# Kernel optimization log

Hardware: AMD Instinct MI355X
Metric: run time of the kernel (lower is better)

## Reference

```python
import jax, jax.numpy as jnp
import numpy as np

N_NODES = 50000
IN_CH = 128
HIDDEN = 64
OUT = 32
HEADS = 4


def _gat_conv(x, src, dst, W, a_src, a_dst, b, heads, ch, concat):
    """PyG-style GATConv (eval mode, self-loops already in src/dst)."""
    N = x.shape[0]
    h = (x @ W).reshape(N, heads, ch)                      # [N,H,C]
    asrc = jnp.einsum('nhc,hc->nh', h, a_src)              # [N,H]
    adst = jnp.einsum('nhc,hc->nh', h, a_dst)              # [N,H]
    e = jax.nn.leaky_relu(asrc[src] + adst[dst], 0.2)      # [E,H]
    # segment softmax over edges grouped by destination node
    m = jax.ops.segment_max(e, dst, num_segments=N)        # [N,H]
    e = jnp.exp(e - m[dst])
    z = jax.ops.segment_sum(e, dst, num_segments=N)        # [N,H]
    alpha = e / (z[dst] + 1e-16)                           # [E,H]
    out = jax.ops.segment_sum(h[src] * alpha[:, :, None], dst, num_segments=N)  # [N,H,C]
    out = out.reshape(N, heads * ch) if concat else out.mean(axis=1)
    return out + b


def _layer_norm(x, g, b):
    mu = x.mean(axis=-1, keepdims=True)
    var = ((x - mu) ** 2).mean(axis=-1, keepdims=True)
    return (x - mu) * jax.lax.rsqrt(var + 1e-5) * g + b


def setup_inputs() -> dict:
    key = jax.random.key(0)
    ks = jax.random.split(key, 20)
    HID = HEADS * HIDDEN  # 256
    s = 0.1
    inp = {
        'x': jax.random.normal(ks[0], (N_NODES, IN_CH), jnp.float32),
        'edge_index': jax.random.randint(ks[1], (2, 800000), 0, N_NODES, jnp.int64 if jax.config.jax_enable_x64 else jnp.int32),
        # conv1
        'W1': jax.random.normal(ks[2], (IN_CH, HID), jnp.float32) * s,
        'a1_src': jax.random.normal(ks[3], (HEADS, HIDDEN), jnp.float32) * s,
        'a1_dst': jax.random.normal(ks[4], (HEADS, HIDDEN), jnp.float32) * s,
        'b1': jnp.zeros((HID,), jnp.float32),
        'g1': jnp.ones((HID,), jnp.float32),
        'be1': jnp.zeros((HID,), jnp.float32),
        # conv2
        'W2': jax.random.normal(ks[5], (HID, HID), jnp.float32) * s,
        'a2_src': jax.random.normal(ks[6], (HEADS, HIDDEN), jnp.float32) * s,
        'a2_dst': jax.random.normal(ks[7], (HEADS, HIDDEN), jnp.float32) * s,
        'b2': jnp.zeros((HID,), jnp.float32),
        'g2': jnp.ones((HID,), jnp.float32),
        'be2': jnp.zeros((HID,), jnp.float32),
        # conv3 (heads=1)
        'W3': jax.random.normal(ks[8], (HID, OUT), jnp.float32) * s,
        'a3_src': jax.random.normal(ks[9], (1, OUT), jnp.float32) * s,
        'a3_dst': jax.random.normal(ks[10], (1, OUT), jnp.float32) * s,
        'b3': jnp.zeros((OUT,), jnp.float32),
    }
    return inp


def reference(x, edge_index, W1, a1_src, a1_dst, b1, g1, be1,
              W2, a2_src, a2_dst, b2, g2, be2,
              W3, a3_src, a3_dst, b3):
    N = x.shape[0]
    loops = jnp.arange(N, dtype=edge_index.dtype)
    ei = jnp.concatenate([edge_index, jnp.stack([loops, loops])], axis=1)
    src, dst = ei[0], ei[1]
    h = _gat_conv(x, src, dst, W1, a1_src, a1_dst, b1, HEADS, HIDDEN, True)
    h = jax.nn.elu(_layer_norm(h, g1, be1))
    h = _gat_conv(h, src, dst, W2, a2_src, a2_dst, b2, HEADS, HIDDEN, True)
    h = jax.nn.elu(_layer_norm(h, g2, be2))
    return _gat_conv(h, src, dst, W3, a3_src, a3_dst, b3, 1, OUT, True)
```

## Files before the change

### kernel.cpp

```cpp
#include <hip/hip_runtime.h>
#include <math.h>

#define NN 50000

typedef __attribute__((ext_vector_type(8))) short bf16x8;
typedef __attribute__((ext_vector_type(4))) float f32x4;

__device__ inline float wred_max(float v){
  #pragma unroll
  for(int s=32;s>0;s>>=1) v=fmaxf(v,__shfl_xor(v,s,64));
  return v;
}
__device__ inline float wred_sum(float v){
  #pragma unroll
  for(int s=32;s>0;s>>=1) v+=__shfl_xor(v,s,64);
  return v;
}
__device__ inline float lrelu(float x){ return x>0.f? x : 0.2f*x; }
__device__ inline float rlf(float v,int l){ return __int_as_float(__builtin_amdgcn_readlane(__float_as_int(v),l)); }

__device__ inline ushort f2bf(float f){
  union{float f;unsigned u;} v; v.f=f;
  unsigned u=v.u;
  return (ushort)((u + 0x7fffu + ((u>>16)&1u)) >> 16);
}
__device__ inline float bflo(unsigned u){ return __uint_as_float(u<<16); }
__device__ inline float bfhi(unsigned u){ return __uint_as_float(u&0xffff0000u); }

__global__ void casttr_k(const float* __restrict__ W, ushort* __restrict__ Wt, int K, int N){
  int i=blockIdx.x*blockDim.x+threadIdx.x;
  if(i<K*N){ int k=i/N, n=i%N; Wt[n*K+k]=f2bf(W[i]); }
}

__global__ void hist_k(const int* __restrict__ dstA,int* __restrict__ counts,int E){
  int i=blockIdx.x*blockDim.x+threadIdx.x;
  if(i<E) atomicAdd(&counts[dstA[i]],1);
}

__global__ __launch_bounds__(1024) void scan1_k(const int* __restrict__ counts,int* __restrict__ offs,
                                                int* __restrict__ bsum,int N){
  __shared__ int stot[16];
  int t=threadIdx.x; int lane=t&63, wv=t>>6;
  int base=blockIdx.x*1024;
  int orig=(base+t<N)?counts[base+t]:0;
  int v=orig;
  #pragma unroll
  for(int s=1;s<64;s<<=1){ int u=__shfl_up(v,s,64); if(lane>=s) v+=u; }
  if(lane==63) stot[wv]=v;
  __syncthreads();
  if(wv==0){
    int tv=(lane<16)?stot[lane]:0;
    #pragma unroll
    for(int s=1;s<16;s<<=1){ int u=__shfl_up(tv,s,64); if(lane>=s) tv+=u; }
    if(lane<16) stot[lane]=tv;
  }
  __syncthreads();
  int wpref=(wv>0)?stot[wv-1]:0;
  if(base+t<N) offs[base+t]=wpref+v-orig;
  if(t==1023) bsum[blockIdx.x]=stot[15];
}
__global__ void scan2_k(int* __restrict__ bsum,int NB){
  int lane=threadIdx.x;
  int v=(lane<NB)?bsum[lane]:0;
  int incl=v;
  #pragma unroll
  for(int s=1;s<64;s<<=1){ int u=__shfl_up(incl,s,64); if(lane>=s) incl+=u; }
  if(lane<NB) bsum[lane]=incl-v;
}
__global__ __launch_bounds__(1024) void scan3_k(int* __restrict__ offs,const int* __restrict__ bsum,int N,int E){
  int i=blockIdx.x*1024+threadIdx.x;
  if(i<N) offs[i]+=bsum[blockIdx.x];
  if(i==N-1) offs[N]=E;
}

__global__ void scatter_k(const int* __restrict__ srcA,const int* __restrict__ dstA,
                          const int* __restrict__ offs,int* cur,int* __restrict__ ssrc,int E){
  int i=blockIdx.x*blockDim.x+threadIdx.x;
  if(i<E){ int d=dstA[i]; int p=offs[d]+atomicAdd(&cur[d],1); ssrc[p]=srcA[i]; }
}

template<int WR,int WC,int MI,int NI,int DOTM,int AF32>
__global__ __launch_bounds__(256,2) void gemm_bf16_k(const void* __restrict__ Av,
    const ushort* __restrict__ Bt, ushort* __restrict__ C,
    const float* __restrict__ aS, const float* __restrict__ aD,
    float* __restrict__ as_, float* __restrict__ ad_,
    int M, int N, int K){
  constexpr int BM = WR*MI*16;
  constexpr int BN = WC*NI*16;
  constexpr int LDK = 40;
  __shared__ ushort sA[BM*LDK];
  __shared__ ushort sB[BN*LDK];
  int tid=threadIdx.x;
  int lane=tid&63, w=tid>>6;
  int wr=w/WC, wc=w%WC;
  int bm=blockIdx.y*BM, bn=blockIdx.x*BN;
  f32x4 acc[MI][NI]={};

  for(int k0=0;k0<K;k0+=32){
    if constexpr (AF32){
      const float* A=(const float*)Av;
      #pragma unroll
      for(int i=0;i<(BM*8)/256;i++){
        int c=tid+i*256;
        int r=c>>3, cc=c&7;
        int gr=bm+r;
        float4 v={0.f,0.f,0.f,0.f};
        if(gr<M) v=*(const float4*)(A+(size_t)gr*K+k0+cc*4);
        unsigned long long p=(unsigned long long)f2bf(v.x)
          |((unsigned long long)f2bf(v.y)<<16)
          |((unsigned long long)f2bf(v.z)<<32)
          |((unsigned long long)f2bf(v.w)<<48);
        *(unsigned long long*)(sA+r*LDK+cc*4)=p;
      }
    } else {
      const ushort* A=(const ushort*)Av;
      #pragma unroll
      for(int i=0;i<(BM*4)/256;i++){
        int c=tid+i*256;
        int r=c>>2, cc=c&3;
        int gr=bm+r;
        ulonglong2 v; v.x=0; v.y=0;
        if(gr<M) v=*(const ulonglong2*)(A+(size_t)gr*K+k0+cc*8);
        *(ulonglong2*)(sA+r*LDK+cc*8)=v;
      }
    }
    if constexpr ((BN*4)>=256){
      #pragma unroll
      for(int i=0;i<(BN*4)/256;i++){
        int c=tid+i*256;
        int r=c>>2, cc=c&3;
        ulonglong2 v=*(const ulonglong2*)(Bt+(size_t)(bn+r)*K+k0+cc*8);
        *(ulonglong2*)(sB+r*LDK+cc*8)=v;
      }
    } else {
      if(tid<BN*4){
        int r=tid>>2, cc=tid&3;
        ulonglong2 v=*(const ulonglong2*)(Bt+(size_t)(bn+r)*K+k0+cc*8);
        *(ulonglong2*)(sB+r*LDK+cc*8)=v;
      }
    }
    __syncthreads();
    bf16x8 af[MI], bf[NI];
    #pragma unroll
    for(int m=0;m<MI;m++)
      af[m]=*(bf16x8*)(sA+((wr*MI+m)*16+(lane&15))*LDK+(lane>>4)*8);
    #pragma unroll
    for(int n=0;n<NI;n++)
      bf[n]=*(bf16x8*)(sB+((wc*NI+n)*16+(lane&15))*LDK+(lane>>4)*8);
    #pragma unroll
    for(int m=0;m<MI;m++)
      #pragma unroll
      for(int n=0;n<NI;n++)
        acc[m][n]=__builtin_amdgcn_mfma_f32_16x16x32_bf16(af[m],bf[n],acc[m][n],0,0,0);
    __syncthreads();
  }
  int rb=lane>>4, cl=lane&15;
  float av[NI], dv[NI];
  #pragma unroll
  for(int n=0;n<NI;n++){
    int gc=bn+(wc*NI+n)*16+cl;
    if constexpr (DOTM!=0){ av[n]=aS[gc]; dv[n]=aD[gc]; }
    else { av[n]=0.f; dv[n]=0.f; }
  }
  #pragma unroll
  for(int m=0;m<MI;m++){
    #pragma unroll
    for(int i=0;i<4;i++){
      int gr=bm+(wr*MI+m)*16+rb*4+i;
      if constexpr (DOTM==1){
        int h=(bn>>6)+wc;
        float ps=0.f,pd=0.f;
        #pragma unroll
        for(int n=0;n<NI;n++){ ps+=acc[m][n][i]*av[n]; pd+=acc[m][n][i]*dv[n]; }
        #pragma unroll
        for(int msk=1;msk<16;msk<<=1){
          ps+=__shfl_xor(ps,msk,64); pd+=__shfl_xor(pd,msk,64);
        }
        if(cl==0 && gr<M){ as_[gr*4+h]=ps; ad_[gr*4+h]=pd; }
      } else if constexpr (DOTM==2){
        float ps=0.f,pd=0.f;
        #pragma unroll
        for(int n=0;n<NI;n++){ ps+=acc[m][n][i]*av[n]; pd+=acc[m][n][i]*dv[n]; }
        #pragma unroll
        for(int msk=1;msk<16;msk<<=1){
          ps+=__shfl_xor(ps,msk,64); pd+=__shfl_xor(pd,msk,64);
        }
        if(cl==0 && gr<M){ as_[gr]=ps; ad_[gr]=pd; }
      }
      if(gr<M){
        #pragma unroll
        for(int n=0;n<NI;n++){
          int gc=bn+(wc*NI+n)*16+cl;
          int pos = (DOTM==1) ? (4*(gc&63)+(gc>>6)) : gc;
          C[(size_t)gr*N+pos]=f2bf(acc[m][n][i]);
        }
      }
    }
  }
}

__global__ __launch_bounds__(256) void agg4_k(const ushort* __restrict__ hb,
    const float* __restrict__ as_,const float* __restrict__ ad_,
    const int* __restrict__ offs,const int* __restrict__ ssrc,
    const float* __restrict__ bias,const float* __restrict__ g,const float* __restrict__ be,
    ushort* __restrict__ outb,int N){
  int lane=threadIdx.x&63, wv=threadIdx.x>>6;
  int n=blockIdx.x*4+wv; if(n>=N) return;
  int lane4=lane*4;
  float ad[4], es[4];
  #pragma unroll
  for(int k=0;k<4;k++) ad[k]=ad_[n*4+k];
  #pragma unroll
  for(int k=0;k<4;k++) es[k]=lrelu(as_[n*4+k]+ad[k]);
  int o0=offs[n],o1=offs[n+1];
  int cnt=o1-o0;
  float m[4], inv[4], acc[4];

  if(cnt<=64){
    int sv=0;
    float lv[4]={-1e30f,-1e30f,-1e30f,-1e30f};
    if(lane<cnt){
      sv=ssrc[o0+lane];
      float4 avv=*(const float4*)(as_+(size_t)sv*4);
      lv[0]=lrelu(avv.x+ad[0]); lv[1]=lrelu(avv.y+ad[1]);
      lv[2]=lrelu(avv.z+ad[2]); lv[3]=lrelu(avv.w+ad[3]);
    }
    #pragma unroll
    for(int k=0;k<4;k++) m[k]=fmaxf(es[k],wred_max(lv[k]));
    float w4[4];
    #pragma unroll
    for(int k=0;k<4;k++) w4[k]=(lane<cnt)?__expf(lv[k]-m[k]):0.f;
    #pragma unroll
    for(int k=0;k<4;k++){
      float z=wred_sum(w4[k])+__expf(es[k]-m[k]);
      inv[k]=1.f/(z+1e-16f);
    }
    #pragma unroll
    for(int k=0;k<4;k++) w4[k]*=inv[k];
    {
      uint2 u=*(const uint2*)(hb+(size_t)n*256+lane4);
      float hv[4]={bflo(u.x),bfhi(u.x),bflo(u.y),bfhi(u.y)};
      #pragma unroll
      for(int k=0;k<4;k++) acc[k]=__expf(es[k]-m[k])*inv[k]*hv[k];
    }
    int cnt8=(cnt+7)&~7;
    uint2 uA[8];
    #pragma unroll
    for(int i=0;i<8;i++){
      int s=__builtin_amdgcn_readlane(sv,i);
      uA[i]=*(const uint2*)(hb+(size_t)s*256+lane4);
    }
    for(int t=0;t<cnt8;t+=8){
      uint2 uB[8];
      if(t+8<cnt8){
        #pragma unroll
        for(int i=0;i<8;i++){
          int s=__builtin_amdgcn_readlane(sv,t+8+i);
          uB[i]=*(const uint2*)(hb+(size_t)s*256+lane4);
        }
      }
      #pragma unroll
      for(int i=0;i<8;i++){
        acc[0]+=rlf(w4[0],t+i)*bflo(uA[i].x);
        acc[1]+=rlf(w4[1],t+i)*bfhi(uA[i].x);
        acc[2]+=rlf(w4[2],t+i)*bflo(uA[i].y);
        acc[3]+=rlf(w4[3],t+i)*bfhi(uA[i].y);
      }
      #pragma unroll
      for(int i=0;i<8;i++) uA[i]=uB[i];
    }
  } else {
    #pragma unroll
    for(int k=0;k<4;k++) m[k]=es[k];
    {
      float lm[4]={-1e30f,-1e30f,-1e30f,-1e30f};
      for(int j=o0+lane;j<o1;j+=64){
        int s=ssrc[j];
        float4 avv=*(const float4*)(as_+(size_t)s*4);
        float a[4]={avv.x,avv.y,avv.z,avv.w};
        #pragma unroll
        for(int k=0;k<4;k++) lm[k]=fmaxf(lm[k],lrelu(a[k]+ad[k]));
      }
      #pragma unroll
      for(int k=0;k<4;k++) m[k]=fmaxf(m[k],wred_max(lm[k]));
    }
    {
      float lz[4]={0.f,0.f,0.f,0.f};
      for(int j=o0+lane;j<o1;j+=64){
        int s=ssrc[j];
        float4 avv=*(const float4*)(as_+(size_t)s*4);
        float a[4]={avv.x,avv.y,avv.z,avv.w};
        #pragma unroll
        for(int k=0;k<4;k++) lz[k]+=__expf(lrelu(a[k]+ad[k])-m[k]);
      }
      #pragma unroll
      for(int k=0;k<4;k++){
        float z=wred_sum(lz[k])+__expf(es[k]-m[k]);
        inv[k]=1.f/(z+1e-16f);
      }
    }
    {
      uint2 u=*(const uint2*)(hb+(size_t)n*256+lane4);
      float hv[4]={bflo(u.x),bfhi(u.x),bflo(u.y),bfhi(u.y)};
      #pragma unroll
      for(int k=0;k<4;k++) acc[k]=__expf(es[k]-m[k])*inv[k]*hv[k];
    }
    for(int base=o0;base<o1;base+=64){
      int c2=min(64,o1-base);
      int j=base+lane;
      int sv=0; float w4[4]={0.f,0.f,0.f,0.f};
      if(j<o1){
        sv=ssrc[j];
        float4 avv=*(const float4*)(as_+(size_t)sv*4);
        float a[4]={avv.x,avv.y,avv.z,avv.w};
        #pragma unroll
        for(int k=0;k<4;k++) w4[k]=__expf(lrelu(a[k]+ad[k])-m[k])*inv[k];
      }
      for(int t=0;t<c2;t++){
        int s=__builtin_amdgcn_readlane(sv,t);
        uint2 u=*(const uint2*)(hb+(size_t)s*256+lane4);
        acc[0]+=rlf(w4[0],t)*bflo(u.x);
        acc[1]+=rlf(w4[1],t)*bfhi(u.x);
        acc[2]+=rlf(w4[2],t)*bflo(u.y);
        acc[3]+=rlf(w4[3],t)*bfhi(u.y);
      }
    }
  }
  #pragma unroll
  for(int k=0;k<4;k++) acc[k]+=bias[k*64+lane];
  float tot=wred_sum(acc[0]+acc[1]+acc[2]+acc[3]);
  float mu=tot*(1.f/256.f);
  float vs=0.f;
  #pragma unroll
  for(int k=0;k<4;k++){ float d=acc[k]-mu; vs+=d*d; }
  float var=wred_sum(vs)*(1.f/256.f);
  float r=rsqrtf(var+1e-5f);
  #pragma unroll
  for(int k=0;k<4;k++){
    float v=(acc[k]-mu)*r*g[k*64+lane]+be[k*64+lane];
    float ev= v>0.f? v : expm1f(v);
    outb[(size_t)n*256+k*64+lane]=f2bf(ev);
  }
}

__global__ __launch_bounds__(256) void agg1_k(const ushort* __restrict__ hb,
    const float* __restrict__ as_,const float* __restrict__ ad_,
    const int* __restrict__ offs,const int* __restrict__ ssrc,
    const float* __restrict__ bias,float* __restrict__ out,int N){
  int lane=threadIdx.x&63, wv=threadIdx.x>>6;
  int n=blockIdx.x*4+wv; if(n>=N) return;
  float ad=ad_[n];
  float es=lrelu(as_[n]+ad);
  int o0=offs[n],o1=offs[n+1];
  int cnt=o1-o0;
  float m, inv, acc=0.f;

  if(cnt<=64){
    int sv=0; float lv=-1e30f;
    if(lane<cnt){ sv=ssrc[o0+lane]; lv=lrelu(as_[sv]+ad); }
    m=fmaxf(es,wred_max(lv));
    float w1=(lane<cnt)?__expf(lv-m):0.f;
    float z=wred_sum(w1)+__expf(es-m);
    inv=1.f/(z+1e-16f);
    w1*=inv;
    if(lane<32) acc=__expf(es-m)*inv*__uint_as_float(((unsigned)hb[(size_t)n*32+lane])<<16);
    int cnt8=(cnt+7)&~7;
    float hA[8];
    #pragma unroll
    for(int i=0;i<8;i++){
      int s=__builtin_amdgcn_readlane(sv,i);
      hA[i]=(lane<32)?__uint_as_float(((unsigned)hb[(size_t)s*32+lane])<<16):0.f;
    }
    for(int t=0;t<cnt8;t+=8){
      float hB[8];
      if(t+8<cnt8){
        #pragma unroll
        for(int i=0;i<8;i++){
          int s=__builtin_amdgcn_readlane(sv,t+8+i);
          hB[i]=(lane<32)?__uint_as_float(((unsigned)hb[(size_t)s*32+lane])<<16):0.f;
        }
      }
      #pragma unroll
      for(int i=0;i<8;i++) acc+=rlf(w1,t+i)*hA[i];
      #pragma unroll
      for(int i=0;i<8;i++) hA[i]=hB[i];
    }
  } else {
    m=es;
    {
      float lm=-1e30f;
      for(int j=o0+lane;j<o1;j+=64) lm=fmaxf(lm,lrelu(as_[ssrc[j]]+ad));
      m=fmaxf(m,wred_max(lm));
    }
    {
      float lz=0.f;
      for(int j=o0+lane;j<o1;j+=64) lz+=__expf(lrelu(as_[ssrc[j]]+ad)-m);
      float z=wred_sum(lz)+__expf(es-m);
      inv=1.f/(z+1e-16f);
    }
    if(lane<32) acc=__expf(es-m)*inv*__uint_as_float(((unsigned)hb[(size_t)n*32+lane])<<16);
    for(int base=o0;base<o1;base+=64){
      int c2=min(64,o1-base);
      int j=base+lane;
      int sv=0; float w1=0.f;
      if(j<o1){ sv=ssrc[j]; w1=__expf(lrelu(as_[sv]+ad)-m)*inv; }
      for(int t=0;t<c2;t++){
        int s=__builtin_amdgcn_readlane(sv,t);
        if(lane<32) acc+=rlf(w1,t)*__uint_as_float(((unsigned)hb[(size_t)s*32+lane])<<16);
      }
    }
  }
  if(lane<32) out[(size_t)n*32+lane]=acc+bias[lane];
}

extern "C" void kernel_launch(void* const* d_in,const int* in_sizes,int n_in,
                              void* d_out,int out_size,void* d_ws,size_t ws_size,
                              hipStream_t stream){
  const float* x  =(const float*)d_in[0];
  const int*   ei =(const int*)  d_in[1];
  const float* W1 =(const float*)d_in[2];
  const float* a1s=(const float*)d_in[3];
  const float* a1d=(const float*)d_in[4];
  const float* b1 =(const float*)d_in[5];
  const float* g1 =(const float*)d_in[6];
  const float* be1=(const float*)d_in[7];
  const float* W2 =(const float*)d_in[8];
  const float* a2s=(const float*)d_in[9];
  const float* a2d=(const float*)d_in[10];
  const float* b2 =(const float*)d_in[11];
  const float* g2 =(const float*)d_in[12];
  const float* be2=(const float*)d_in[13];
  const float* W3 =(const float*)d_in[14];
  const float* a3s=(const float*)d_in[15];
  const float* a3d=(const float*)d_in[16];
  const float* b3 =(const float*)d_in[17];
  float* outp=(float*)d_out;
  int N=NN;
  int E=in_sizes[1]/2;
  const int* srcA=ei;
  const int* dstA=ei+E;

  char* w=(char*)d_ws;
  ushort* hb =(ushort*)w; w+=(size_t)N*256*2;
  ushort* h3b=(ushort*)w; w+=(size_t)N*32*2;
  ushort* obb=(ushort*)w; w+=(size_t)N*256*2;
  ushort* w1t=(ushort*)w; w+=(size_t)256*128*2;
  ushort* w2t=(ushort*)w; w+=(size_t)256*256*2;
  ushort* w3t=(ushort*)w; w+=(size_t)32*256*2;
  float* asb =(float*)w; w+=(size_t)N*4*4;
  float* adb =(float*)w; w+=(size_t)N*4*4;
  int* offs=(int*)w; w+=(size_t)(N+4)*4;
  int* cur =(int*)w; w+=(size_t)N*4;
  int* ssrc=(int*)w; w+=(size_t)E*4;
  int* bsum=(int*)w; w+=(size_t)64*4;

  int NB=(N+1023)/1024;

  hipMemsetAsync(cur,0,(size_t)N*4,stream);
  hist_k<<<(E+255)/256,256,0,stream>>>(dstA,cur,E);
  scan1_k<<<NB,1024,0,stream>>>(cur,offs,bsum,N);
  scan2_k<<<1,64,0,stream>>>(bsum,NB);
  scan3_k<<<NB,1024,0,stream>>>(offs,bsum,N,E);
  hipMemsetAsync(cur,0,(size_t)N*4,stream);
  scatter_k<<<(E+255)/256,256,0,stream>>>(srcA,dstA,offs,cur,ssrc,E);

  casttr_k<<<(128*256+255)/256,256,0,stream>>>(W1,w1t,128,256);
  casttr_k<<<(256*256+255)/256,256,0,stream>>>(W2,w2t,256,256);
  casttr_k<<<(256*32+255)/256,256,0,stream>>>(W3,w3t,256,32);

  int nblkN=(N+3)/4;
  int gY128=(N+127)/128;

  gemm_bf16_k<2,2,4,4,1,1><<<dim3(2,gY128),256,0,stream>>>(x,w1t,hb,a1s,a1d,asb,adb,N,256,128);
  agg4_k<<<nblkN,256,0,stream>>>(hb,asb,adb,offs,ssrc,b1,g1,be1,obb,N);

  gemm_bf16_k<2,2,4,4,1,0><<<dim3(2,gY128),256,0,stream>>>(obb,w2t,hb,a2s,a2d,asb,adb,N,256,256);
  agg4_k<<<nblkN,256,0,stream>>>(hb,asb,adb,offs,ssrc,b2,g2,be2,obb,N);

  gemm_bf16_k<4,1,2,2,2,0><<<dim3(1,gY128),256,0,stream>>>(obb,w3t,h3b,a3s,a3d,asb,adb,N,32,256);
  agg1_k<<<nblkN,256,0,stream>>>(h3b,asb,adb,offs,ssrc,b3,outp,N);
}
```

Before: 360.6 us.

## Merge scan kernels, stage attention weights in LDS, split agg1 edges across half-waves

Removes the separate block-sum scan launch by having each scan3 block sum the preceding block totals itself with a wave reduction. In agg4 the per-edge softmax weights go into shared memory and are read from there, replacing readlane broadcasts, and the software-pipelined double buffer of neighbor loads becomes a plain batch of eight loads per iteration. In agg1 the two half-waves each take alternate edges so all 64 lanes do work, with a final cross-half shuffle to combine the sums. The risks are less overlap of memory latency in agg4 and extra LDS traffic.

New measurement: 344.8 us. 4.4% less time.

```diff
diff --git a/kernel.cpp b/kernel.cpp
--- a/kernel.cpp
+++ b/kernel.cpp
@@ -59,17 +59,18 @@
   if(base+t<N) offs[base+t]=wpref+v-orig;
   if(t==1023) bsum[blockIdx.x]=stot[15];
 }
-__global__ void scan2_k(int* __restrict__ bsum,int NB){
-  int lane=threadIdx.x;
-  int v=(lane<NB)?bsum[lane]:0;
-  int incl=v;
-  #pragma unroll
-  for(int s=1;s<64;s<<=1){ int u=__shfl_up(incl,s,64); if(lane>=s) incl+=u; }
-  if(lane<NB) bsum[lane]=incl-v;
-}
 __global__ __launch_bounds__(1024) void scan3_k(int* __restrict__ offs,const int* __restrict__ bsum,int N,int E){
-  int i=blockIdx.x*1024+threadIdx.x;
-  if(i<N) offs[i]+=bsum[blockIdx.x];
+  __shared__ int sbase;
+  int t=threadIdx.x;
+  if(t<64){
+    int v=(t<(int)blockIdx.x)?bsum[t]:0;
+    #pragma unroll
+    for(int s=32;s>0;s>>=1) v+=__shfl_xor(v,s,64);
+    if(t==0) sbase=v;
+  }
+  __syncthreads();
+  int i=blockIdx.x*1024+t;
+  if(i<N) offs[i]+=sbase;
   if(i==N-1) offs[N]=E;
 }
 
@@ -204,6 +205,7 @@
     const int* __restrict__ offs,const int* __restrict__ ssrc,
     const float* __restrict__ bias,const float* __restrict__ g,const float* __restrict__ be,
     ushort* __restrict__ outb,int N){
+  __shared__ float wlds[4][64][4];
   int lane=threadIdx.x&63, wv=threadIdx.x>>6;
   int n=blockIdx.x*4+wv; if(n>=N) return;
   int lane4=lane*4;
@@ -237,37 +239,31 @@
     }
     #pragma unroll
     for(int k=0;k<4;k++) w4[k]*=inv[k];
+    *(float4*)&wlds[wv][lane][0]=make_float4(w4[0],w4[1],w4[2],w4[3]);
+    asm volatile("s_waitcnt lgkmcnt(0)":::"memory");
     {
       uint2 u=*(const uint2*)(hb+(size_t)n*256+lane4);
       float hv[4]={bflo(u.x),bfhi(u.x),bflo(u.y),bfhi(u.y)};
       #pragma unroll
       for(int k=0;k<4;k++) acc[k]=__expf(es[k]-m[k])*inv[k]*hv[k];
     }
-    int cnt8=(cnt+7)&~7;
-    uint2 uA[8];
-    #pragma unroll
-    for(int i=0;i<8;i++){
-      int s=__builtin_amdgcn_readlane(sv,i);
-      uA[i]=*(const uint2*)(hb+(size_t)s*256+lane4);
-    }
-    for(int t=0;t<cnt8;t+=8){
-      uint2 uB[8];
-      if(t+8<cnt8){
-        #pragma unroll
-        for(int i=0;i<8;i++){
-          int s=__builtin_amdgcn_readlane(sv,t+8+i);
-          uB[i]=*(const uint2*)(hb+(size_t)s*256+lane4);
-        }
-      }
+    int nbat=(cnt+7)>>3;
+    for(int b=0;b<nbat;b++){
+      int e0=b*8;
+      uint2 u[8];
       #pragma unroll
       for(int i=0;i<8;i++){
-        acc[0]+=rlf(w4[0],t+i)*bflo(uA[i].x);
-        acc[1]+=rlf(w4[1],t+i)*bfhi(uA[i].x);
-        acc[2]+=rlf(w4[2],t+i)*bflo(uA[i].y);
-        acc[3]+=rlf(w4[3],t+i)*bfhi(uA[i].y);
-      }
-      #pragma unroll
-      for(int i=0;i<8;i++) uA[i]=uB[i];
+        int s=__builtin_amdgcn_readlane(sv,e0+i);
+        u[i]=*(const uint2*)(hb+((size_t)s<<8)+lane4);
+      }
+      #pragma unroll
+      for(int i=0;i<8;i++){
+        const float* wp=&wlds[wv][e0+i][0];
+        acc[0]+=wp[0]*bflo(u[i].x);
+        acc[1]+=wp[1]*bfhi(u[i].x);
+        acc[2]+=wp[2]*bflo(u[i].y);
+        acc[3]+=wp[3]*bfhi(u[i].y);
+      }
     }
   } else {
     #pragma unroll
@@ -354,6 +350,8 @@
   int o0=offs[n],o1=offs[n+1];
   int cnt=o1-o0;
   float m, inv, acc=0.f;
+  int lane32=lane&31;
+  int half=lane>>5;
 
   if(cnt<=64){
     int sv=0; float lv=-1e30f;
@@ -363,28 +361,18 @@
     float z=wred_sum(w1)+__expf(es-m);
     inv=1.f/(z+1e-16f);
     w1*=inv;
-    if(lane<32) acc=__expf(es-m)*inv*__uint_as_float(((unsigned)hb[(size_t)n*32+lane])<<16);
-    int cnt8=(cnt+7)&~7;
-    float hA[8];
-    #pragma unroll
-    for(int i=0;i<8;i++){
-      int s=__builtin_amdgcn_readlane(sv,i);
-      hA[i]=(lane<32)?__uint_as_float(((unsigned)hb[(size_t)s*32+lane])<<16):0.f;
-    }
-    for(int t=0;t<cnt8;t+=8){
-      float hB[8];
-      if(t+8<cnt8){
-        #pragma unroll
-        for(int i=0;i<8;i++){
-          int s=__builtin_amdgcn_readlane(sv,t+8+i);
-          hB[i]=(lane<32)?__uint_as_float(((unsigned)hb[(size_t)s*32+lane])<<16):0.f;
-        }
-      }
-      #pragma unroll
-      for(int i=0;i<8;i++) acc+=rlf(w1,t+i)*hA[i];
-      #pragma unroll
-      for(int i=0;i<8;i++) hA[i]=hB[i];
-    }
+    if(half==0) acc=__expf(es-m)*inv*__uint_as_float(((unsigned)hb[(size_t)n*32+lane32])<<16);
+    int cnt2=(cnt+1)&~1;
+    for(int t=0;t<cnt2;t+=2){
+      int sL=__builtin_amdgcn_readlane(sv,t);
+      int sH=__builtin_amdgcn_readlane(sv,t+1);
+      float wL=rlf(w1,t), wH=rlf(w1,t+1);
+      int s = half? sH : sL;
+      float ww = half? wH : wL;
+      float hv=__uint_as_float(((unsigned)hb[(size_t)s*32+lane32])<<16);
+      acc+=ww*hv;
+    }
+    acc+=__shfl_xor(acc,32,64);
   } else {
     m=es;
     {
@@ -459,7 +447,6 @@
   hipMemsetAsync(cur,0,(size_t)N*4,stream);
   hist_k<<<(E+255)/256,256,0,stream>>>(dstA,cur,E);
   scan1_k<<<NB,1024,0,stream>>>(cur,offs,bsum,N);
-  scan2_k<<<1,64,0,stream>>>(bsum,NB);
   scan3_k<<<NB,1024,0,stream>>>(offs,bsum,N,E);
   hipMemsetAsync(cur,0,(size_t)N*4,stream);
   scatter_k<<<(E+255)/256,256,0,stream>>>(srcA,dstA,offs,cur,ssrc,E);
```
